# Kernel tuning notes

Hardware: AMD Instinct MI355X
Metric: run time of the kernel (lower is better)

The kernel has to match this reference:

```python
import jax, jax.numpy as jnp
import numpy as np

B, L, D = 4, 2048, 1024
H, DK, DV, CS = 4, 128, 256, 16  # heads, head_qk_dim, head_v_dim, chunk_size
KD, VD = H * DK, H * DV          # 512, 1024
CONV = 4
EPS = 1e-5


def silu(x):
    return x * jax.nn.sigmoid(x)


def setup_inputs():
    key = jax.random.key(0)
    ks = jax.random.split(key, 9)
    s = 0.02
    return {
        "hidden_states": jax.random.normal(ks[0], (B, L, D), jnp.float32),
        "conv_w": jax.random.normal(ks[1], (D, CONV), jnp.float32) * 0.2,
        "Wq": jax.random.normal(ks[2], (KD, D), jnp.float32) * s,
        "Wk": jax.random.normal(ks[3], (KD, D), jnp.float32) * s,
        "Wv": jax.random.normal(ks[4], (VD, D), jnp.float32) * s,
        "Wb": jax.random.normal(ks[5], (H, D), jnp.float32) * s,
        "Wg": jax.random.normal(ks[6], (VD, D), jnp.float32) * s,
        "Wo": jax.random.normal(ks[7], (D, VD), jnp.float32) * s,
        "norm_w": jnp.ones((DV,), jnp.float32),
    }


def short_conv(x, w):
    # causal depthwise conv1d with SiLU activation: x [B,L,D], w [D,K]
    K = w.shape[1]
    xp = jnp.pad(x, ((0, 0), (K - 1, 0), (0, 0)))
    y = sum(xp[:, j:j + x.shape[1], :] * w[:, j] for j in range(K))
    return silu(y)


def delta_rule_chunk(q, k, v, beta):
    # fused_chunk_delta_rule: q,k [B,H,L,DK], v [B,H,L,DV], beta [B,H,L]
    b, h, l, dk = q.shape
    dv = v.shape[-1]
    nc = l // CS
    k = k * jax.lax.rsqrt(jnp.sum(k * k, -1, keepdims=True) + 1e-12)  # L2-normalize keys
    q = q * (dk ** -0.5)
    qc = q.reshape(b, h, nc, CS, dk)
    kc = k.reshape(b, h, nc, CS, dk)
    vc = v.reshape(b, h, nc, CS, dv)
    bc = beta.reshape(b, h, nc, CS)
    kb = kc * bc[..., None]
    # WY representation: T = (I + strict_tril(diag(beta) K K^T))^{-1}
    A = jnp.einsum('bhncd,bhnmd->bhncm', kb, kc)
    strict = jnp.tril(jnp.ones((CS, CS), q.dtype), -1)
    M = jnp.eye(CS, dtype=q.dtype) + A * strict
    eye = jnp.broadcast_to(jnp.eye(CS, dtype=q.dtype), M.shape)
    T = jax.scipy.linalg.solve_triangular(M, eye, lower=True)
    w = jnp.einsum('bhncm,bhnmd->bhncd', T, kb)
    u = jnp.einsum('bhncm,bhnmd->bhncd', T, vc * bc[..., None])
    causal = jnp.tril(jnp.ones((CS, CS), q.dtype))

    def step(S, inp):
        qi, ki, wi, ui = inp  # [B,H,CS,dk/dv]
        u_adj = ui - jnp.einsum('bhcd,bhdv->bhcv', wi, S)
        attn = jnp.einsum('bhcd,bhmd->bhcm', qi, ki) * causal
        o = jnp.einsum('bhcd,bhdv->bhcv', qi, S) + jnp.einsum('bhcm,bhmv->bhcv', attn, u_adj)
        S = S + jnp.einsum('bhcd,bhcv->bhdv', ki, u_adj)
        return S, o

    xs = tuple(jnp.moveaxis(t, 2, 0) for t in (qc, kc, w, u))
    S0 = jnp.zeros((b, h, dk, dv), q.dtype)
    _, os_ = jax.lax.scan(step, S0, xs)
    return jnp.moveaxis(os_, 0, 2).reshape(b, h, l, dv)


def reference(hidden_states, conv_w, Wq, Wk, Wv, Wb, Wg, Wo, norm_w):
    x = short_conv(hidden_states, conv_w)
    q = (x @ Wq.T).reshape(B, L, H, DK).transpose(0, 2, 1, 3)
    k = (x @ Wk.T).reshape(B, L, H, DK).transpose(0, 2, 1, 3)
    v = (x @ Wv.T).reshape(B, L, H, DV).transpose(0, 2, 1, 3)
    beta = jax.nn.sigmoid(x @ Wb.T).transpose(0, 2, 1)  # [B,H,L]
    o = delta_rule_chunk(q, k, v, beta)                 # [B,H,L,DV]
    o = o.transpose(0, 2, 1, 3)                          # [B,L,H,DV]
    g = (x @ Wg.T).reshape(B, L, H, DV)
    o = o * jax.lax.rsqrt(jnp.mean(o * o, -1, keepdims=True) + EPS) * norm_w * silu(g)
    return o.reshape(B, L, VD) @ Wo.T
```

## Files before the change

kernel.cpp:

```cpp
#include <hip/hip_runtime.h>
#include <cstdint>
#include <cstddef>

typedef _Float16 f16;
typedef _Float16 f16x4 __attribute__((ext_vector_type(4)));
typedef _Float16 f16x8 __attribute__((ext_vector_type(8)));
typedef float floatx4 __attribute__((ext_vector_type(4)));

#define MFMA32(a,b,c) __builtin_amdgcn_mfma_f32_16x16x32_f16((a),(b),(c),0,0,0)

#define ROWS 8192
#define NCHUNK 128
static constexpr float QSCALE = 0.08838834764831845f;

static __device__ __forceinline__ float sigmoidf_(float x) { return 1.0f / (1.0f + expf(-x)); }

static __device__ __forceinline__ uint32_t pack2(f16 a, f16 b) {
  union { f16 h[2]; uint32_t u; } v; v.h[0] = a; v.h[1] = b; return v.u;
}

#define GLOAD_LDS(gptr, lptr)                                                  \
  __builtin_amdgcn_global_load_lds(                                            \
      (const __attribute__((address_space(1))) void*)(gptr),                   \
      (__attribute__((address_space(3))) void*)(lptr), 16, 0, 0)

#define WAITV(N) do { asm volatile("s_waitcnt vmcnt(" #N ")" ::: "memory");    \
                      __builtin_amdgcn_sched_barrier(0); } while (0)

#define SBAR() __builtin_amdgcn_sched_barrier(0)

__global__ __launch_bounds__(256) void wconv_kernel(
    const float* __restrict__ Wq, const float* __restrict__ Wk,
    const float* __restrict__ Wv, const float* __restrict__ Wg,
    const float* __restrict__ Wo,
    f16* __restrict__ WcatHi, f16* __restrict__ WcatLoKV, f16* __restrict__ WoHi) {
  int tid = blockIdx.x * 256 + threadIdx.x;
  int e8 = tid * 8;
  if (e8 < 3145728) {
    int row = e8 >> 10, col = e8 & 1023;
    const float* src;
    if (row < 512)       src = Wk + (size_t)row * 1024 + col;
    else if (row < 1536) src = Wv + (size_t)(row - 512) * 1024 + col;
    else if (row < 2048) src = Wq + (size_t)(row - 1536) * 1024 + col;
    else                 src = Wg + (size_t)(row - 2048) * 1024 + col;
    f16 thi[8] __attribute__((aligned(16)));
    f16 tlo[8] __attribute__((aligned(16)));
#pragma unroll
    for (int j = 0; j < 8; j++) {
      float x = src[j];
      f16 h = (f16)x;
      thi[j] = h;
      tlo[j] = (f16)(x - (float)h);
    }
    *(uint4*)&WcatHi[e8] = *(const uint4*)thi;
    if (row < 1536) *(uint4*)&WcatLoKV[e8] = *(const uint4*)tlo;
  } else {
    int idx = e8 - 3145728;
    f16 t[8] __attribute__((aligned(16)));
#pragma unroll
    for (int j = 0; j < 8; j++) t[j] = (f16)Wo[idx + j];
    *(uint4*)&WoHi[idx] = *(const uint4*)t;
  }
}

__global__ __launch_bounds__(256) void conv_kernel(
    const float* __restrict__ hs, const float* __restrict__ cw,
    f16* __restrict__ xhi, f16* __restrict__ xlo) {
  int row = blockIdx.x;
  int b = row >> 11, l = row & 2047;
  int d = threadIdx.x * 4;
  floatx4 w0 = *(const floatx4*)&cw[(d + 0) * 4];
  floatx4 w1 = *(const floatx4*)&cw[(d + 1) * 4];
  floatx4 w2 = *(const floatx4*)&cw[(d + 2) * 4];
  floatx4 w3 = *(const floatx4*)&cw[(d + 3) * 4];
  floatx4 acc = {0.f, 0.f, 0.f, 0.f};
#pragma unroll
  for (int j = 0; j < 4; j++) {
    int ls = l - 3 + j;
    if (ls < 0) continue;
    floatx4 hv = *(const floatx4*)&hs[(size_t)(b * 2048 + ls) * 1024 + d];
    acc[0] += hv[0] * w0[j];
    acc[1] += hv[1] * w1[j];
    acc[2] += hv[2] * w2[j];
    acc[3] += hv[3] * w3[j];
  }
  f16 ohi[4] __attribute__((aligned(8)));
  f16 olo[4] __attribute__((aligned(8)));
#pragma unroll
  for (int q = 0; q < 4; q++) {
    float y = acc[q] * sigmoidf_(acc[q]);
    f16 h = (f16)y;
    ohi[q] = h;
    olo[q] = (f16)(y - (float)h);
  }
  *(uint2*)&xhi[(size_t)row * 1024 + d] = *(const uint2*)ohi;
  *(uint2*)&xlo[(size_t)row * 1024 + d] = *(const uint2*)olo;
}

__global__ __launch_bounds__(256) void beta_kernel(
    const f16* __restrict__ xhi, const f16* __restrict__ xlo,
    const float* __restrict__ Wb, float* __restrict__ betaf) {
  int row = blockIdx.x;
  int t = threadIdx.x;
  __shared__ floatx4 red[256];
  int c = t * 4;
  float xv[4];
#pragma unroll
  for (int j = 0; j < 4; j++)
    xv[j] = (float)xhi[(size_t)row * 1024 + c + j] + (float)xlo[(size_t)row * 1024 + c + j];
  floatx4 p = {0.f, 0.f, 0.f, 0.f};
#pragma unroll
  for (int hh = 0; hh < 4; hh++) {
    const float* wr = Wb + hh * 1024 + c;
    p[hh] = xv[0] * wr[0] + xv[1] * wr[1] + xv[2] * wr[2] + xv[3] * wr[3];
  }
  red[t] = p;
  __syncthreads();
  for (int s = 128; s > 0; s >>= 1) {
    if (t < s) red[t] += red[t + s];
    __syncthreads();
  }
  if (t < 4) betaf[(size_t)row * 4 + t] = sigmoidf_(red[0][t]);
}

__global__ __launch_bounds__(256) void gemm_hilo_kv(
    const f16* __restrict__ Ahi, const f16* __restrict__ Alo,
    const f16* __restrict__ Bhi, const f16* __restrict__ Blo,
    f16* __restrict__ ChHi, f16* __restrict__ ChLo, int K) {
  __shared__ __attribute__((aligned(16))) f16 AsH[4096];
  __shared__ __attribute__((aligned(16))) f16 AsL[4096];
  __shared__ __attribute__((aligned(16))) f16 BsH[4096];
  __shared__ __attribute__((aligned(16))) f16 BsL[4096];
  const int t = threadIdx.x;
  const int lane = t & 63, wave = t >> 6;
  const int lc = lane & 15, quad = lane >> 4;
  const int wm = (wave >> 1) * 64, wn = (wave & 1) * 64;
  const int m0 = blockIdx.y * 128, n0 = blockIdx.x * 128;
  const int scol = ((lane & 3) ^ ((lane >> 3) & 3)) * 8;
  int srow[2];
#pragma unroll
  for (int pp = 0; pp < 2; pp++) srow[pp] = (wave * 2 + pp) * 16 + (lane >> 2);
  const int swz = (quad ^ ((lc >> 1) & 3)) * 8;
  floatx4 acc[4][4] = {};
  for (int kt = 0; kt < K; kt += 32) {
    __syncthreads();
#pragma unroll
    for (int pp = 0; pp < 2; pp++) {
      int ldso = (wave * 2 + pp) * 512;
      GLOAD_LDS(&Ahi[(size_t)(m0 + srow[pp]) * K + kt + scol], AsH + ldso);
      GLOAD_LDS(&Alo[(size_t)(m0 + srow[pp]) * K + kt + scol], AsL + ldso);
      GLOAD_LDS(&Bhi[(size_t)(n0 + srow[pp]) * K + kt + scol], BsH + ldso);
      GLOAD_LDS(&Blo[(size_t)(n0 + srow[pp]) * K + kt + scol], BsL + ldso);
    }
    __syncthreads();
    f16x8 ah[4], al[4], bh2[4], bl[4];
#pragma unroll
    for (int i = 0; i < 4; i++) {
      ah[i] = *(const f16x8*)&AsH[(wm + i * 16 + lc) * 32 + swz];
      al[i] = *(const f16x8*)&AsL[(wm + i * 16 + lc) * 32 + swz];
    }
#pragma unroll
    for (int j = 0; j < 4; j++) {
      bh2[j] = *(const f16x8*)&BsH[(wn + j * 16 + lc) * 32 + swz];
      bl[j]  = *(const f16x8*)&BsL[(wn + j * 16 + lc) * 32 + swz];
    }
#pragma unroll
    for (int i = 0; i < 4; i++)
#pragma unroll
      for (int j = 0; j < 4; j++) {
        acc[i][j] = MFMA32(ah[i], bh2[j], acc[i][j]);
        acc[i][j] = MFMA32(al[i], bh2[j], acc[i][j]);
        acc[i][j] = MFMA32(ah[i], bl[j], acc[i][j]);
      }
  }
#pragma unroll
  for (int i = 0; i < 4; i++)
#pragma unroll
    for (int j = 0; j < 4; j++)
#pragma unroll
      for (int rr = 0; rr < 4; rr++) {
        int row = m0 + wm + i * 16 + quad * 4 + rr;
        int col = n0 + wn + j * 16 + lc;
        float x = acc[i][j][rr];
        f16 h = (f16)x;
        ChHi[(size_t)row * 3072 + col] = h;
        ChLo[(size_t)row * 1536 + col] = (f16)(x - (float)h);
      }
}

template <int OUTF16>
__global__ __launch_bounds__(256) void gemm_plain(
    const f16* __restrict__ A, const f16* __restrict__ Bw,
    f16* __restrict__ Ch, float* __restrict__ Cf, int K, int ldc) {
  __shared__ __attribute__((aligned(16))) f16 As[4096];
  __shared__ __attribute__((aligned(16))) f16 Bs[4096];
  const int t = threadIdx.x;
  const int lane = t & 63, wave = t >> 6;
  const int lc = lane & 15, quad = lane >> 4;
  const int wm = (wave >> 1) * 64, wn = (wave & 1) * 64;
  const int m0 = blockIdx.y * 128, n0 = blockIdx.x * 128;
  const int scol = ((lane & 3) ^ ((lane >> 3) & 3)) * 8;
  int srow[2];
#pragma unroll
  for (int pp = 0; pp < 2; pp++) srow[pp] = (wave * 2 + pp) * 16 + (lane >> 2);
  const int swz = (quad ^ ((lc >> 1) & 3)) * 8;
  floatx4 acc[4][4] = {};
  for (int kt = 0; kt < K; kt += 32) {
    __syncthreads();
#pragma unroll
    for (int pp = 0; pp < 2; pp++) {
      int ldso = (wave * 2 + pp) * 512;
      GLOAD_LDS(&A[(size_t)(m0 + srow[pp]) * K + kt + scol],  As + ldso);
      GLOAD_LDS(&Bw[(size_t)(n0 + srow[pp]) * K + kt + scol], Bs + ldso);
    }
    __syncthreads();
    f16x8 af[4], bf[4];
#pragma unroll
    for (int i = 0; i < 4; i++) af[i] = *(const f16x8*)&As[(wm + i * 16 + lc) * 32 + swz];
#pragma unroll
    for (int j = 0; j < 4; j++) bf[j] = *(const f16x8*)&Bs[(wn + j * 16 + lc) * 32 + swz];
#pragma unroll
    for (int i = 0; i < 4; i++)
#pragma unroll
      for (int j = 0; j < 4; j++) acc[i][j] = MFMA32(af[i], bf[j], acc[i][j]);
  }
#pragma unroll
  for (int i = 0; i < 4; i++)
#pragma unroll
    for (int j = 0; j < 4; j++)
#pragma unroll
      for (int rr = 0; rr < 4; rr++) {
        int row = m0 + wm + i * 16 + quad * 4 + rr;
        int col = n0 + wn + j * 16 + lc;
        if (OUTF16) Ch[(size_t)row * ldc + col] = (f16)acc[i][j][rr];
        else        Cf[(size_t)row * ldc + col] = acc[i][j][rr];
      }
}

__global__ __launch_bounds__(256) void prepass_kernel(
    const f16* __restrict__ qkvgHi, const f16* __restrict__ kvLo,
    const float* __restrict__ betaf,
    f16* __restrict__ wHi, f16* __restrict__ wLo,
    f16* __restrict__ kTHi, f16* __restrict__ kTLo,
    f16* __restrict__ uHi, f16* __restrict__ uLo,
    float* __restrict__ attno) {
  int bid = blockIdx.x;
  int bh = bid >> 7, n = bid & 127;
  int b = bh >> 2, h = bh & 3;
  int t = threadIdx.x;

  __shared__ __attribute__((aligned(16))) float kc[16][132];
  __shared__ __attribute__((aligned(16))) float qc[16][132];
  __shared__ __attribute__((aligned(16))) float vb[16][260];
  __shared__ float Mm[16][16];
  __shared__ float Tt[16][16];
  __shared__ float Tb[16][16];
  __shared__ float part[16][16];
  __shared__ float betas[16];
  __shared__ float nrm[16];

  const size_t rowbase = (size_t)(b * 2048 + n * 16);
  {
    int i = t >> 4, o8 = (t & 15) * 8;
    size_t oh = (rowbase + i) * 3072;
    size_t ol = (rowbase + i) * 1536;
#pragma unroll
    for (int j = 0; j < 8; j++)
      kc[i][o8 + j] = (float)qkvgHi[oh + h * 128 + o8 + j] +
                      (float)kvLo[ol + h * 128 + o8 + j];
#pragma unroll
    for (int j = 0; j < 8; j++)
      qc[i][o8 + j] = (float)qkvgHi[oh + 1536 + h * 128 + o8 + j];
  }
  if (t < 16) betas[t] = betaf[(rowbase + t) * 4 + h];
  __syncthreads();
  {
    int i = t >> 4, sg = t & 15;
    float s = 0.f;
#pragma unroll
    for (int j = 0; j < 8; j++) { float v = kc[i][sg * 8 + j]; s += v * v; }
    part[i][sg] = s;
  }
  __syncthreads();
  if (t < 16) {
    float s = 0.f;
#pragma unroll
    for (int j = 0; j < 16; j++) s += part[t][j];
    nrm[t] = rsqrtf(s + 1e-12f);
  }
  __syncthreads();
  {
    int i = t >> 4, o8 = (t & 15) * 8;
    float sc = nrm[i];
#pragma unroll
    for (int j = 0; j < 8; j++) kc[i][o8 + j] *= sc;
  }
  __syncthreads();
  {
    int d = t & 127, ih = t >> 7;
    f16 thi[8] __attribute__((aligned(16)));
    f16 tlo[8] __attribute__((aligned(16)));
#pragma unroll
    for (int j = 0; j < 8; j++) {
      float x = kc[ih * 8 + j][d];
      f16 hh = (f16)x;
      thi[j] = hh;
      tlo[j] = (f16)(x - (float)hh);
    }
    size_t base = ((size_t)bh * 128 + n) * 2048 + d * 16 + ih * 8;
    *(uint4*)&kTHi[base] = *(const uint4*)thi;
    *(uint4*)&kTLo[base] = *(const uint4*)tlo;
  }
  {
    int i = t >> 4, j = t & 15;
    float s = 0.f;
    for (int x = 0; x < 128; x += 4)
      s += kc[i][x] * kc[j][x] + kc[i][x + 1] * kc[j][x + 1] +
           kc[i][x + 2] * kc[j][x + 2] + kc[i][x + 3] * kc[j][x + 3];
    Mm[i][j] = (i == j ? 1.f : 0.f) + ((j < i) ? betas[i] * s : 0.f);
  }
  __syncthreads();
  if (t < 16) {
    int j = t;
    float Tc[16];
#pragma unroll
    for (int i = 0; i < 16; i++) Tc[i] = 0.f;
    Tc[j] = 1.f;
    for (int i = j + 1; i < 16; i++) {
      float s = 0.f;
      for (int k2 = j; k2 < i; k2++) s += Mm[i][k2] * Tc[k2];
      Tc[i] = -s;
    }
    for (int i = 0; i < 16; i++) Tt[i][j] = Tc[i];
  }
  __syncthreads();
  { int i = t >> 4, m = t & 15; Tb[i][m] = Tt[i][m] * betas[m]; }
  {
    int m = t >> 4, c16 = (t & 15) * 16;
    size_t oh = (rowbase + m) * 3072 + 512 + h * 256 + c16;
    size_t ol = (rowbase + m) * 1536 + 512 + h * 256 + c16;
    float bm = betas[m];
#pragma unroll
    for (int j = 0; j < 16; j++)
      vb[m][c16 + j] = bm * ((float)qkvgHi[oh + j] + (float)kvLo[ol + j]);
  }
  __syncthreads();
  {
    int i = t >> 4, dg = t & 15;
    f16 thi[8] __attribute__((aligned(16)));
    f16 tlo[8] __attribute__((aligned(16)));
#pragma unroll
    for (int dd = 0; dd < 8; dd++) {
      int d = dg * 8 + dd;
      float s = 0.f;
#pragma unroll
      for (int m = 0; m < 16; m++) s += Tb[i][m] * kc[m][d];
      s = -s;
      f16 hh = (f16)s;
      thi[dd] = hh;
      tlo[dd] = (f16)(s - (float)hh);
    }
    size_t base = ((size_t)bh * 128 + n) * 2048 + i * 128 + dg * 8;
    *(uint4*)&wHi[base] = *(const uint4*)thi;
    *(uint4*)&wLo[base] = *(const uint4*)tlo;
  }
  {
    int v = t;
    f16 thi[16] __attribute__((aligned(16)));
    f16 tlo[16] __attribute__((aligned(16)));
#pragma unroll
    for (int i = 0; i < 16; i++) {
      float s2 = 0.f;
#pragma unroll
      for (int m = 0; m < 16; m++) s2 += Tt[i][m] * vb[m][v];
      f16 hh = (f16)s2;
      thi[i] = hh;
      tlo[i] = (f16)(s2 - (float)hh);
    }
    size_t base = ((((size_t)(v >> 4) * 16 + bh) * 128 + n) * 16 + (v & 15)) * 16;
    ((uint4*)&uHi[base])[0] = ((const uint4*)thi)[0];
    ((uint4*)&uHi[base])[1] = ((const uint4*)thi)[1];
    ((uint4*)&uLo[base])[0] = ((const uint4*)tlo)[0];
    ((uint4*)&uLo[base])[1] = ((const uint4*)tlo)[1];
  }
  {
    int i = t >> 4, j = t & 15;
    float s = 0.f;
    for (int x = 0; x < 128; x++) s += qc[i][x] * kc[j][x];
    attno[((size_t)bh * 128 + n) * 256 + i * 16 + j] = (j <= i) ? QSCALE * s : 0.f;
  }
}

#define STG_W   0
#define STG_WL  2048
#define STG_Q   4096
#define STG_KH  6144
#define STG_KL  8192
#define STG_SZ  10240

__global__ __launch_bounds__(64, 1) void scan_kernel(
    const f16* __restrict__ qkvgHi,
    const f16* __restrict__ wHi, const f16* __restrict__ wLo,
    const f16* __restrict__ kTHi, const f16* __restrict__ kTLo,
    const float* __restrict__ attn,
    const f16* __restrict__ uHi, const f16* __restrict__ uLo,
    float* __restrict__ o1, float* __restrict__ o2) {
  const int bid = blockIdx.x;
  const int slc = bid & 15, bh = bid >> 4;
  const int b = bh >> 2, h = bh & 3;
  const int v0 = slc * 16;
  const int lane = threadIdx.x;
  const int lc = lane & 15, quad = lane >> 4;
  const int qh = quad & 1;

  __shared__ __attribute__((aligned(16))) f16 stg[2][STG_SZ];
  __shared__ __attribute__((aligned(16))) f16 S_hi[16][136];
  __shared__ __attribute__((aligned(16))) f16 S_lo[16][136];

  floatx4 accS[8] = {};

  const size_t cb = (size_t)bh * 128;
  const f16* qb = qkvgHi + (size_t)b * 2048 * 3072 + 1536 + h * 128;
  const f16* ubH = uHi + ((size_t)(slc * 16 + bh)) * 128 * 256 + lc * 16 + quad * 4;
  const f16* ubL = uLo + ((size_t)(slc * 16 + bh)) * 128 * 256 + lc * 16 + quad * 4;
  const float* ab = attn + cb * 256 + lc * 16 + qh * 8;
  float* ob = (bh < 12) ? (o1 + (size_t)bh * 2048 * 256)
                        : (o2 + (size_t)(bh - 12) * 2048 * 256);

  int woff[4], koff[4], qoff[4];
#pragma unroll
  for (int p = 0; p < 4; p++) {
    int cid = p * 64 + lane;
    int row = cid >> 4, dgs = (cid & 15) ^ (row & 7);
    int d = cid >> 1,  ih = (cid & 1) ^ ((cid >> 3) & 1);
    woff[p] = row * 128 + dgs * 8;
    koff[p] = d * 16 + ih * 8;
    qoff[p] = row * 3072 + dgs * 8;
  }

  uint4 pa0[2], pa1[2];
  uint2 puh[2], pul[2];

  auto ISSUE_REG = [&](int slot, int nn) {
    pa0[slot] = *(const uint4*)(ab + (size_t)nn * 256);
    pa1[slot] = *(const uint4*)(ab + (size_t)nn * 256 + 4);
    puh[slot] = *(const uint2*)(ubH + (size_t)nn * 256);
    pul[slot] = *(const uint2*)(ubL + (size_t)nn * 256);
  };
  auto ISSUE_WQ = [&](int buf, int nn) {
    const f16* wsrc  = wHi + (cb + (size_t)nn) * 2048;
    const f16* wlsrc = wLo + (cb + (size_t)nn) * 2048;
    const f16* qsrc  = qb + (size_t)nn * 16 * 3072;
    f16* sbp = &stg[buf][0];
#pragma unroll
    for (int p = 0; p < 4; p++) {
      GLOAD_LDS(wsrc + woff[p],  sbp + STG_W  + p * 512);
      GLOAD_LDS(wlsrc + woff[p], sbp + STG_WL + p * 512);
      GLOAD_LDS(qsrc + qoff[p],  sbp + STG_Q  + p * 512);
    }
  };
  auto ISSUE_K = [&](int buf, int nn) {
    const f16* khsrc = kTHi + (cb + (size_t)nn) * 2048;
    const f16* klsrc = kTLo + (cb + (size_t)nn) * 2048;
    f16* sbp = &stg[buf][0];
#pragma unroll
    for (int p = 0; p < 4; p++) {
      GLOAD_LDS(khsrc + koff[p], sbp + STG_KH + p * 512);
      GLOAD_LDS(klsrc + koff[p], sbp + STG_KL + p * 512);
    }
  };

  ISSUE_REG(0, 0); ISSUE_WQ(0, 0); ISSUE_K(0, 0);
  SBAR();
  ISSUE_REG(1, 1); ISSUE_WQ(1, 1); ISSUE_K(1, 1);

  for (int n = 0; n < NCHUNK; n += 2) {
#pragma unroll
    for (int hf = 0; hf < 2; hf++) {
      const int nn = n + hf;
      f16* sb = &stg[hf][0];

#pragma unroll
      for (int dt = 0; dt < 8; dt++) {
        f16x4 h4, l4;
#pragma unroll
        for (int r = 0; r < 4; r++) {
          float x = accS[dt][r];
          f16 hh = (f16)x;
          h4[r] = hh;
          l4[r] = (f16)(x - (float)hh);
        }
        *(f16x4*)&S_hi[lc][dt * 16 + quad * 4] = h4;
        *(f16x4*)&S_lo[lc][dt * 16 + quad * 4] = l4;
      }

      if (nn == 0)       WAITV(24);
      else if (nn == 1)  WAITV(28);
      else if (nn < 127) WAITV(32);
      else               WAITV(8);

      floatx4 acc_u;
      {
        union { uint2 u2; f16 hh[4]; } Uh, Ul;
        Uh.u2 = puh[hf]; Ul.u2 = pul[hf];
#pragma unroll
        for (int r = 0; r < 4; r++) acc_u[r] = (float)Uh.hh[r] + (float)Ul.hh[r];
      }
      f16x8 aah, aal;
      {
        union { uint4 u4[2]; float f[8]; } PA;
        PA.u4[0] = pa0[hf]; PA.u4[1] = pa1[hf];
#pragma unroll
        for (int j = 0; j < 8; j++) {
          float a = PA.f[j];
          f16 ahh = (f16)a;
          aah[j] = ahh;
          aal[j] = (f16)(a - (float)ahh);
        }
      }
      if (nn + 2 < NCHUNK) ISSUE_REG(hf, nn + 2);

      f16x8 shf[4], slf[4], wah[4], wal[4], qah[4];
#pragma unroll
      for (int ks = 0; ks < 4; ks++) {
        shf[ks] = *(const f16x8*)&S_hi[lc][ks * 32 + quad * 8];
        slf[ks] = *(const f16x8*)&S_lo[lc][ks * 32 + quad * 8];
        int gi = lc * 128 + (((ks * 4 + quad) ^ (lc & 7)) * 8);
        wah[ks] = *(const f16x8*)(sb + STG_W  + gi);
        wal[ks] = *(const f16x8*)(sb + STG_WL + gi);
        qah[ks] = *(const f16x8*)(sb + STG_Q  + gi);
      }
      SBAR();
      if (nn + 2 < NCHUNK) ISSUE_WQ(hf, nn + 2);

      floatx4 a1 = {0.f, 0.f, 0.f, 0.f}, a2 = {0.f, 0.f, 0.f, 0.f};
#pragma unroll
      for (int ks = 0; ks < 4; ks++) {
        acc_u = MFMA32(wah[ks], shf[ks], acc_u);
        a1    = MFMA32(wah[ks], slf[ks], a1);
        a2    = MFMA32(wal[ks], shf[ks], a2);
      }
      acc_u = acc_u + a1 + a2;

      f16x8 ubf;
      {
        f16 h0 = (f16)acc_u[0], h1 = (f16)acc_u[1];
        f16 h2 = (f16)acc_u[2], h3 = (f16)acc_u[3];
        uint32_t uh01 = pack2(h0, h1), uh23 = pack2(h2, h3);
        uint32_t ul01 = pack2((f16)(acc_u[0] - (float)h0), (f16)(acc_u[1] - (float)h1));
        uint32_t ul23 = pack2((f16)(acc_u[2] - (float)h2), (f16)(acc_u[3] - (float)h3));
        int srcA = (2 * qh) * 16 + lc;
        int srcB = srcA + 16;
        uint32_t Ah0 = __shfl((int)uh01, srcA, 64), Ah1 = __shfl((int)uh23, srcA, 64);
        uint32_t Bh0 = __shfl((int)uh01, srcB, 64), Bh1 = __shfl((int)uh23, srcB, 64);
        uint32_t Al0 = __shfl((int)ul01, srcA, 64), Al1 = __shfl((int)ul23, srcA, 64);
        uint32_t Bl0 = __shfl((int)ul01, srcB, 64), Bl1 = __shfl((int)ul23, srcB, 64);
        union { uint32_t u[4]; f16x8 v; } U;
        bool hi = (quad < 2);
        U.u[0] = hi ? Ah0 : Al0;
        U.u[1] = hi ? Ah1 : Al1;
        U.u[2] = hi ? Bh0 : Bl0;
        U.u[3] = hi ? Bh1 : Bl1;
        ubf = U.v;
      }

      const int kswz = (qh ^ ((lc >> 2) & 1)) * 8 + lc * 16;
#pragma unroll
      for (int dt = 0; dt < 8; dt++) {
        f16x8 kah = *(const f16x8*)(sb + STG_KH + dt * 256 + kswz);
        f16x8 kal = *(const f16x8*)(sb + STG_KL + dt * 256 + kswz);
        accS[dt] = MFMA32(kah, ubf, accS[dt]);
        accS[dt] = MFMA32(kal, ubf, accS[dt]);
      }
      SBAR();
      if (nn + 2 < NCHUNK) ISSUE_K(hf, nn + 2);
      SBAR();

      floatx4 acc_o = {0.f, 0.f, 0.f, 0.f};
#pragma unroll
      for (int ks = 0; ks < 4; ks++) acc_o = MFMA32(qah[ks], shf[ks], acc_o);
#pragma unroll
      for (int ks = 0; ks < 4; ks++) acc_o = MFMA32(qah[ks], slf[ks], acc_o);
#pragma unroll
      for (int r = 0; r < 4; r++) acc_o[r] *= QSCALE;
      acc_o = MFMA32(aah, ubf, acc_o);
      acc_o = MFMA32(aal, ubf, acc_o);
#pragma unroll
      for (int r = 0; r < 4; r++)
        ob[(size_t)(nn * 16 + quad * 4 + r) * 256 + v0 + lc] = acc_o[r];
    }
  }
}

__global__ __launch_bounds__(256) void gate_kernel(
    const float* __restrict__ o1, const float* __restrict__ o2,
    const f16* __restrict__ qkvgHi, const float* __restrict__ norm_w,
    f16* __restrict__ onh) {
  int h = threadIdx.x >> 6, lane = threadIdx.x & 63;
  int r = blockIdx.x;
  int b = r >> 11, l = r & 2047;
  int bh = b * 4 + h;
  const float* orow = ((bh < 12) ? (o1 + (size_t)bh * 524288)
                                 : (o2 + (size_t)(bh - 12) * 524288)) + (size_t)l * 256;
  int v = lane * 4;
  floatx4 ov = *(const floatx4*)&orow[v];
  float ss = ov[0] * ov[0] + ov[1] * ov[1] + ov[2] * ov[2] + ov[3] * ov[3];
  for (int m = 32; m > 0; m >>= 1) ss += __shfl_xor(ss, m);
  float rms = rsqrtf(ss * (1.0f / 256.0f) + 1e-5f);
  size_t goff = (size_t)r * 3072 + 2048 + h * 256 + v;
  floatx4 nw = *(const floatx4*)&norm_w[v];
  f16 outv[4] __attribute__((aligned(8)));
#pragma unroll
  for (int q2 = 0; q2 < 4; q2++) {
    float g = (float)qkvgHi[goff + q2];
    outv[q2] = (f16)(ov[q2] * rms * nw[q2] * (g * sigmoidf_(g)));
  }
  *(uint2*)&onh[(size_t)r * 1024 + h * 256 + v] = *(const uint2*)outv;
}

extern "C" void kernel_launch(void* const* d_in, const int* in_sizes, int n_in,
                              void* d_out, int out_size, void* d_ws, size_t ws_size,
                              hipStream_t stream) {
  (void)in_sizes; (void)n_in; (void)out_size; (void)ws_size;
  const float* hs     = (const float*)d_in[0];
  const float* conv_w = (const float*)d_in[1];
  const float* Wq     = (const float*)d_in[2];
  const float* Wk     = (const float*)d_in[3];
  const float* Wv     = (const float*)d_in[4];
  const float* Wb     = (const float*)d_in[5];
  const float* Wg     = (const float*)d_in[6];
  const float* Wo     = (const float*)d_in[7];
  const float* norm_w = (const float*)d_in[8];
  float* out = (float*)d_out;

  char* ws = (char*)d_ws;
  f16*   x_hi    = (f16*)(ws + 0);
  f16*   x_lo    = (f16*)(ws + 16777216);
  f16*   uHi     = (f16*)(ws + 0);
  f16*   uLo     = (f16*)(ws + 16777216);
  f16*   WcatHi  = (f16*)(ws + 33554432);
  float* o2f     = (float*)(ws + 33554432);
  f16*   WcatLo  = (f16*)(ws + 39845888);
  f16*   WoHi    = (f16*)(ws + 42991616);
  float* betaf   = (float*)(ws + 45088768);
  f16*   qkvgHi  = (f16*)(ws + 45219840);
  f16*   kvLo    = (f16*)(ws + 95551488);
  float* o1f     = (float*)(ws + 95551488);
  f16*   wHi     = (f16*)(ws + 120717312);
  f16*   on_h    = (f16*)(ws + 120717312);
  f16*   wLo     = (f16*)(ws + 129105920);
  f16*   kTHi    = (f16*)(ws + 137494528);
  f16*   kTLo    = (f16*)(ws + 145883136);
  float* attnf   = (float*)(ws + 154271744);

  wconv_kernel<<<2048, 256, 0, stream>>>(Wq, Wk, Wv, Wg, Wo, WcatHi, WcatLo, WoHi);
  conv_kernel<<<ROWS, 256, 0, stream>>>(hs, conv_w, x_hi, x_lo);
  beta_kernel<<<ROWS, 256, 0, stream>>>(x_hi, x_lo, Wb, betaf);
  gemm_hilo_kv<<<dim3(12, 64), 256, 0, stream>>>(
      x_hi, x_lo, WcatHi, WcatLo, qkvgHi, kvLo, 1024);
  gemm_plain<1><<<dim3(12, 64), 256, 0, stream>>>(
      x_hi, WcatHi + (size_t)1536 * 1024, qkvgHi + 1536, nullptr, 1024, 3072);
  prepass_kernel<<<16 * NCHUNK, 256, 0, stream>>>(
      qkvgHi, kvLo, betaf, wHi, wLo, kTHi, kTLo, uHi, uLo, attnf);
  scan_kernel<<<256, 64, 0, stream>>>(
      qkvgHi, wHi, wLo, kTHi, kTLo, attnf, uHi, uLo, o1f, o2f);
  gate_kernel<<<ROWS, 256, 0, stream>>>(o1f, o2f, qkvgHi, norm_w, on_h);
  gemm_plain<0><<<dim3(8, 64), 256, 0, stream>>>(
      on_h, WoHi, nullptr, out, 1024, 1024);
}
```

Baseline: 590.3 us.

## Process two value-column slices per scan wavefront to reuse staged W, Q, K tiles

Each scan block now handles two 16-wide value slices (v0 and v0+128) instead of one, halving the grid to 128 single-wave blocks. The staged W, Q and K tiles and the attention matrix are loaded once and feed two independent MFMA chains, which also gives more instruction-level parallelism inside the serial chunk recurrence. The output computation moves before the state update, and one barrier per chunk is removed. The cost is fewer blocks (128 on a 256-CU part), more registers per wave, and a longer serial path per block.

Result: slower. 676.2 us (+14.6%).

```diff
diff --git a/kernel.cpp b/kernel.cpp
--- a/kernel.cpp
+++ b/kernel.cpp
@@ -406,23 +406,25 @@
     const f16* __restrict__ uHi, const f16* __restrict__ uLo,
     float* __restrict__ o1, float* __restrict__ o2) {
   const int bid = blockIdx.x;
-  const int slc = bid & 15, bh = bid >> 4;
+  const int bh = bid & 15, sp = bid >> 4;
   const int b = bh >> 2, h = bh & 3;
-  const int v0 = slc * 16;
+  const int v0a = sp * 16, v0b = sp * 16 + 128;
   const int lane = threadIdx.x;
   const int lc = lane & 15, quad = lane >> 4;
   const int qh = quad & 1;
 
   __shared__ __attribute__((aligned(16))) f16 stg[2][STG_SZ];
-  __shared__ __attribute__((aligned(16))) f16 S_hi[16][136];
-  __shared__ __attribute__((aligned(16))) f16 S_lo[16][136];
-
-  floatx4 accS[8] = {};
+  __shared__ __attribute__((aligned(16))) f16 S_hi[2][16][136];
+  __shared__ __attribute__((aligned(16))) f16 S_lo[2][16][136];
+
+  floatx4 accS0[8] = {}, accS1[8] = {};
 
   const size_t cb = (size_t)bh * 128;
   const f16* qb = qkvgHi + (size_t)b * 2048 * 3072 + 1536 + h * 128;
-  const f16* ubH = uHi + ((size_t)(slc * 16 + bh)) * 128 * 256 + lc * 16 + quad * 4;
-  const f16* ubL = uLo + ((size_t)(slc * 16 + bh)) * 128 * 256 + lc * 16 + quad * 4;
+  const f16* ubH0 = uHi + ((size_t)(sp * 16 + bh)) * 32768 + lc * 16 + quad * 4;
+  const f16* ubL0 = uLo + ((size_t)(sp * 16 + bh)) * 32768 + lc * 16 + quad * 4;
+  const f16* ubH1 = uHi + ((size_t)((sp + 8) * 16 + bh)) * 32768 + lc * 16 + quad * 4;
+  const f16* ubL1 = uLo + ((size_t)((sp + 8) * 16 + bh)) * 32768 + lc * 16 + quad * 4;
   const float* ab = attn + cb * 256 + lc * 16 + qh * 8;
   float* ob = (bh < 12) ? (o1 + (size_t)bh * 2048 * 256)
                         : (o2 + (size_t)(bh - 12) * 2048 * 256);
@@ -439,13 +441,15 @@
   }
 
   uint4 pa0[2], pa1[2];
-  uint2 puh[2], pul[2];
+  uint2 puh0[2], pul0[2], puh1[2], pul1[2];
 
   auto ISSUE_REG = [&](int slot, int nn) {
-    pa0[slot] = *(const uint4*)(ab + (size_t)nn * 256);
-    pa1[slot] = *(const uint4*)(ab + (size_t)nn * 256 + 4);
-    puh[slot] = *(const uint2*)(ubH + (size_t)nn * 256);
-    pul[slot] = *(const uint2*)(ubL + (size_t)nn * 256);
+    pa0[slot]  = *(const uint4*)(ab + (size_t)nn * 256);
+    pa1[slot]  = *(const uint4*)(ab + (size_t)nn * 256 + 4);
+    puh0[slot] = *(const uint2*)(ubH0 + (size_t)nn * 256);
+    pul0[slot] = *(const uint2*)(ubL0 + (size_t)nn * 256);
+    puh1[slot] = *(const uint2*)(ubH1 + (size_t)nn * 256);
+    pul1[slot] = *(const uint2*)(ubL1 + (size_t)nn * 256);
   };
   auto ISSUE_WQ = [&](int buf, int nn) {
     const f16* wsrc  = wHi + (cb + (size_t)nn) * 2048;
@@ -470,6 +474,27 @@
     }
   };
 
+  auto SHFL_EXCH = [&](floatx4 acc_u) -> f16x8 {
+    f16 h0 = (f16)acc_u[0], h1 = (f16)acc_u[1];
+    f16 h2 = (f16)acc_u[2], h3 = (f16)acc_u[3];
+    uint32_t uh01 = pack2(h0, h1), uh23 = pack2(h2, h3);
+    uint32_t ul01 = pack2((f16)(acc_u[0] - (float)h0), (f16)(acc_u[1] - (float)h1));
+    uint32_t ul23 = pack2((f16)(acc_u[2] - (float)h2), (f16)(acc_u[3] - (float)h3));
+    int srcA = (2 * qh) * 16 + lc;
+    int srcB = srcA + 16;
+    uint32_t Ah0 = __shfl((int)uh01, srcA, 64), Ah1 = __shfl((int)uh23, srcA, 64);
+    uint32_t Bh0 = __shfl((int)uh01, srcB, 64), Bh1 = __shfl((int)uh23, srcB, 64);
+    uint32_t Al0 = __shfl((int)ul01, srcA, 64), Al1 = __shfl((int)ul23, srcA, 64);
+    uint32_t Bl0 = __shfl((int)ul01, srcB, 64), Bl1 = __shfl((int)ul23, srcB, 64);
+    union { uint32_t u[4]; f16x8 v; } U;
+    bool hi = (quad < 2);
+    U.u[0] = hi ? Ah0 : Al0;
+    U.u[1] = hi ? Ah1 : Al1;
+    U.u[2] = hi ? Bh0 : Bl0;
+    U.u[3] = hi ? Bh1 : Bl1;
+    return U.v;
+  };
+
   ISSUE_REG(0, 0); ISSUE_WQ(0, 0); ISSUE_K(0, 0);
   SBAR();
   ISSUE_REG(1, 1); ISSUE_WQ(1, 1); ISSUE_K(1, 1);
@@ -482,29 +507,37 @@
 
 #pragma unroll
       for (int dt = 0; dt < 8; dt++) {
-        f16x4 h4, l4;
+        f16x4 h4a, l4a, h4b, l4b;
 #pragma unroll
         for (int r = 0; r < 4; r++) {
-          float x = accS[dt][r];
-          f16 hh = (f16)x;
-          h4[r] = hh;
-          l4[r] = (f16)(x - (float)hh);
+          float x0 = accS0[dt][r];
+          f16 hh0 = (f16)x0;
+          h4a[r] = hh0;
+          l4a[r] = (f16)(x0 - (float)hh0);
+          float x1 = accS1[dt][r];
+          f16 hh1 = (f16)x1;
+          h4b[r] = hh1;
+          l4b[r] = (f16)(x1 - (float)hh1);
         }
-        *(f16x4*)&S_hi[lc][dt * 16 + quad * 4] = h4;
-        *(f16x4*)&S_lo[lc][dt * 16 + quad * 4] = l4;
-      }
-
-      if (nn == 0)       WAITV(24);
-      else if (nn == 1)  WAITV(28);
-      else if (nn < 127) WAITV(32);
+        *(f16x4*)&S_hi[0][lc][dt * 16 + quad * 4] = h4a;
+        *(f16x4*)&S_lo[0][lc][dt * 16 + quad * 4] = l4a;
+        *(f16x4*)&S_hi[1][lc][dt * 16 + quad * 4] = h4b;
+        *(f16x4*)&S_lo[1][lc][dt * 16 + quad * 4] = l4b;
+      }
+
+      if (nn == 0)       WAITV(26);
+      else if (nn < 127) WAITV(34);
       else               WAITV(8);
 
-      floatx4 acc_u;
+      floatx4 acc_u0, acc_u1;
       {
         union { uint2 u2; f16 hh[4]; } Uh, Ul;
-        Uh.u2 = puh[hf]; Ul.u2 = pul[hf];
-#pragma unroll
-        for (int r = 0; r < 4; r++) acc_u[r] = (float)Uh.hh[r] + (float)Ul.hh[r];
+        Uh.u2 = puh0[hf]; Ul.u2 = pul0[hf];
+#pragma unroll
+        for (int r = 0; r < 4; r++) acc_u0[r] = (float)Uh.hh[r] + (float)Ul.hh[r];
+        Uh.u2 = puh1[hf]; Ul.u2 = pul1[hf];
+#pragma unroll
+        for (int r = 0; r < 4; r++) acc_u1[r] = (float)Uh.hh[r] + (float)Ul.hh[r];
       }
       f16x8 aah, aal;
       {
@@ -520,11 +553,13 @@
       }
       if (nn + 2 < NCHUNK) ISSUE_REG(hf, nn + 2);
 
-      f16x8 shf[4], slf[4], wah[4], wal[4], qah[4];
+      f16x8 shf0[4], slf0[4], shf1[4], slf1[4], wah[4], wal[4], qah[4];
 #pragma unroll
       for (int ks = 0; ks < 4; ks++) {
-        shf[ks] = *(const f16x8*)&S_hi[lc][ks * 32 + quad * 8];
-        slf[ks] = *(const f16x8*)&S_lo[lc][ks * 32 + quad * 8];
+        shf0[ks] = *(const f16x8*)&S_hi[0][lc][ks * 32 + quad * 8];
+        slf0[ks] = *(const f16x8*)&S_lo[0][lc][ks * 32 + quad * 8];
+        shf1[ks] = *(const f16x8*)&S_hi[1][lc][ks * 32 + quad * 8];
+        slf1[ks] = *(const f16x8*)&S_lo[1][lc][ks * 32 + quad * 8];
         int gi = lc * 128 + (((ks * 4 + quad) ^ (lc & 7)) * 8);
         wah[ks] = *(const f16x8*)(sb + STG_W  + gi);
         wal[ks] = *(const f16x8*)(sb + STG_WL + gi);
@@ -533,35 +568,45 @@
       SBAR();
       if (nn + 2 < NCHUNK) ISSUE_WQ(hf, nn + 2);
 
-      floatx4 a1 = {0.f, 0.f, 0.f, 0.f}, a2 = {0.f, 0.f, 0.f, 0.f};
+      floatx4 a10 = {0.f,0.f,0.f,0.f}, a20 = {0.f,0.f,0.f,0.f};
+      floatx4 a11 = {0.f,0.f,0.f,0.f}, a21 = {0.f,0.f,0.f,0.f};
 #pragma unroll
       for (int ks = 0; ks < 4; ks++) {
-        acc_u = MFMA32(wah[ks], shf[ks], acc_u);
-        a1    = MFMA32(wah[ks], slf[ks], a1);
-        a2    = MFMA32(wal[ks], shf[ks], a2);
-      }
-      acc_u = acc_u + a1 + a2;
-
-      f16x8 ubf;
-      {
-        f16 h0 = (f16)acc_u[0], h1 = (f16)acc_u[1];
-        f16 h2 = (f16)acc_u[2], h3 = (f16)acc_u[3];
-        uint32_t uh01 = pack2(h0, h1), uh23 = pack2(h2, h3);
-        uint32_t ul01 = pack2((f16)(acc_u[0] - (float)h0), (f16)(acc_u[1] - (float)h1));
-        uint32_t ul23 = pack2((f16)(acc_u[2] - (float)h2), (f16)(acc_u[3] - (float)h3));
-        int srcA = (2 * qh) * 16 + lc;
-        int srcB = srcA + 16;
-        uint32_t Ah0 = __shfl((int)uh01, srcA, 64), Ah1 = __shfl((int)uh23, srcA, 64);
-        uint32_t Bh0 = __shfl((int)uh01, srcB, 64), Bh1 = __shfl((int)uh23, srcB, 64);
-        uint32_t Al0 = __shfl((int)ul01, srcA, 64), Al1 = __shfl((int)ul23, srcA, 64);
-        uint32_t Bl0 = __shfl((int)ul01, srcB, 64), Bl1 = __shfl((int)ul23, srcB, 64);
-        union { uint32_t u[4]; f16x8 v; } U;
-        bool hi = (quad < 2);
-        U.u[0] = hi ? Ah0 : Al0;
-        U.u[1] = hi ? Ah1 : Al1;
-        U.u[2] = hi ? Bh0 : Bl0;
-        U.u[3] = hi ? Bh1 : Bl1;
-        ubf = U.v;
+        acc_u0 = MFMA32(wah[ks], shf0[ks], acc_u0);
+        acc_u1 = MFMA32(wah[ks], shf1[ks], acc_u1);
+        a10    = MFMA32(wah[ks], slf0[ks], a10);
+        a11    = MFMA32(wah[ks], slf1[ks], a11);
+        a20    = MFMA32(wal[ks], shf0[ks], a20);
+        a21    = MFMA32(wal[ks], shf1[ks], a21);
+      }
+      acc_u0 = acc_u0 + a10 + a20;
+      acc_u1 = acc_u1 + a11 + a21;
+
+      floatx4 acc_o0 = {0.f,0.f,0.f,0.f}, acc_o1 = {0.f,0.f,0.f,0.f};
+#pragma unroll
+      for (int ks = 0; ks < 4; ks++) {
+        acc_o0 = MFMA32(qah[ks], shf0[ks], acc_o0);
+        acc_o1 = MFMA32(qah[ks], shf1[ks], acc_o1);
+      }
+#pragma unroll
+      for (int ks = 0; ks < 4; ks++) {
+        acc_o0 = MFMA32(qah[ks], slf0[ks], acc_o0);
+        acc_o1 = MFMA32(qah[ks], slf1[ks], acc_o1);
+      }
+
+      f16x8 ubf0 = SHFL_EXCH(acc_u0);
+      f16x8 ubf1 = SHFL_EXCH(acc_u1);
+
+#pragma unroll
+      for (int r = 0; r < 4; r++) { acc_o0[r] *= QSCALE; acc_o1[r] *= QSCALE; }
+      acc_o0 = MFMA32(aah, ubf0, acc_o0);
+      acc_o1 = MFMA32(aah, ubf1, acc_o1);
+      acc_o0 = MFMA32(aal, ubf0, acc_o0);
+      acc_o1 = MFMA32(aal, ubf1, acc_o1);
+#pragma unroll
+      for (int r = 0; r < 4; r++) {
+        ob[(size_t)(nn * 16 + quad * 4 + r) * 256 + v0a + lc] = acc_o0[r];
+        ob[(size_t)(nn * 16 + quad * 4 + r) * 256 + v0b + lc] = acc_o1[r];
       }
 
       const int kswz = (qh ^ ((lc >> 2) & 1)) * 8 + lc * 16;
@@ -569,25 +614,13 @@
       for (int dt = 0; dt < 8; dt++) {
         f16x8 kah = *(const f16x8*)(sb + STG_KH + dt * 256 + kswz);
         f16x8 kal = *(const f16x8*)(sb + STG_KL + dt * 256 + kswz);
-        accS[dt] = MFMA32(kah, ubf, accS[dt]);
-        accS[dt] = MFMA32(kal, ubf, accS[dt]);
+        accS0[dt] = MFMA32(kah, ubf0, accS0[dt]);
+        accS1[dt] = MFMA32(kah, ubf1, accS1[dt]);
+        accS0[dt] = MFMA32(kal, ubf0, accS0[dt]);
+        accS1[dt] = MFMA32(kal, ubf1, accS1[dt]);
       }
       SBAR();
       if (nn + 2 < NCHUNK) ISSUE_K(hf, nn + 2);
-      SBAR();
-
-      floatx4 acc_o = {0.f, 0.f, 0.f, 0.f};
-#pragma unroll
-      for (int ks = 0; ks < 4; ks++) acc_o = MFMA32(qah[ks], shf[ks], acc_o);
-#pragma unroll
-      for (int ks = 0; ks < 4; ks++) acc_o = MFMA32(qah[ks], slf[ks], acc_o);
-#pragma unroll
-      for (int r = 0; r < 4; r++) acc_o[r] *= QSCALE;
-      acc_o = MFMA32(aah, ubf, acc_o);
-      acc_o = MFMA32(aal, ubf, acc_o);
-#pragma unroll
-      for (int r = 0; r < 4; r++)
-        ob[(size_t)(nn * 16 + quad * 4 + r) * 256 + v0 + lc] = acc_o[r];
     }
   }
 }
@@ -662,7 +695,7 @@
       x_hi, WcatHi + (size_t)1536 * 1024, qkvgHi + 1536, nullptr, 1024, 3072);
   prepass_kernel<<<16 * NCHUNK, 256, 0, stream>>>(
       qkvgHi, kvLo, betaf, wHi, wLo, kTHi, kTLo, uHi, uLo, attnf);
-  scan_kernel<<<256, 64, 0, stream>>>(
+  scan_kernel<<<128, 64, 0, stream>>>(
       qkvgHi, wHi, wLo, kTHi, kTLo, attnf, uHi, uLo, o1f, o2f);
   gate_kernel<<<ROWS, 256, 0, stream>>>(o1f, o2f, qkvgHi, norm_w, on_h);
   gemm_plain<0><<<dim3(8, 64), 256, 0, stream>>>(
```
